# Kernel tuning notes

Measured on AMD Instinct MI355X. Metric: run time of the kernel, lower is better.

Reference implementation:

```python
import jax, jax.numpy as jnp
import numpy as np

IN_FEATURES = 4096
OUT_FEATURES = 768
N_BITS = 8
BATCH = 4096


def setup_inputs() -> dict:
    key = jax.random.key(0)
    k1, k2, k3 = jax.random.split(key, 3)
    latent = jax.random.uniform(k1, (BATCH, IN_FEATURES), dtype=jnp.float32)
    true_sum = jax.random.uniform(k2, (BATCH, OUT_FEATURES * N_BITS), dtype=jnp.float32)
    # kaiming-normal-ish init: std = sqrt(2 / fan_in)
    weight = jax.random.normal(k3, (IN_FEATURES, OUT_FEATURES * N_BITS), dtype=jnp.float32) * np.sqrt(2.0 / IN_FEATURES)
    return {"latent": latent, "true_sum": true_sum, "weight": weight, "n_bits": N_BITS}


def reference(latent, true_sum, weight, n_bits):
    in_features = weight.shape[0]
    batch = latent.shape[0]
    # powers of two, MSB negated (two's-complement style decode)
    powers = (2.0 ** jnp.arange(n_bits, dtype=jnp.float32))
    powers = powers.at[-1].multiply(-1.0)

    prob_weights = jax.nn.sigmoid(weight)                      # [in, out*n_bits]
    # decode soft bits -> integer-valued weights: [in, out]
    int_weights = (prob_weights.reshape(in_features, -1, n_bits) * powers).sum(-1)
    # decode target bits -> integer-valued sums: [batch, out]
    int_sum = (true_sum.reshape(batch, -1, n_bits) * powers).sum(-1)

    # (latent.unsqueeze(-1) * int_weights).sum(-2) is exactly a GEMM
    pred = latent @ int_weights                                # [batch, out]

    scale_factor = 2.0 ** (n_bits - 1)
    recon_loss = jnp.mean((pred - int_sum) ** 2) / scale_factor
    polarize_loss = jnp.mean(prob_weights * (1.0 - prob_weights))
    return (recon_loss, polarize_loss)
```

## Files before the change

kernel.cpp:

```cpp
#include <hip/hip_runtime.h>
#include <stdint.h>

#define IN_F   4096
#define OUT_F  768
#define NB     8
#define BATCH  4096
#define WCOLS  (OUT_F*NB)

typedef short  bf16x8  __attribute__((ext_vector_type(8)));
typedef float  f32x4   __attribute__((ext_vector_type(4)));
typedef unsigned short ushort8 __attribute__((ext_vector_type(8)));

__device__ __forceinline__ unsigned short f2bf(float f){
    union { float f; uint32_t u; } v; v.f = f;
    uint32_t u = v.u;
    u += 0x7FFFu + ((u >> 16) & 1u);
    return (unsigned short)(u >> 16);
}

__device__ __forceinline__ float bf2f(unsigned short u){
    union { uint32_t q; float f; } v; v.q = ((uint32_t)u) << 16;
    return v.f;
}

__device__ __forceinline__ void gload16(const void* g, void* l){
    __builtin_amdgcn_global_load_lds(
        (const __attribute__((address_space(1))) unsigned int*)g,
        (__attribute__((address_space(3))) unsigned int*)l, 16, 0, 0);
}

#define WAITV(n) do {                                                   \
    asm volatile("s_waitcnt vmcnt(" #n ")" ::: "memory");               \
    __builtin_amdgcn_sched_barrier(0);                                  \
} while (0)

__global__ void prep_latent(const float* __restrict__ lat,
                            unsigned short* __restrict__ abf,
                            float* __restrict__ acc){
    if (blockIdx.x == 0 && threadIdx.x < 4) acc[threadIdx.x] = 0.f;
    int idx = (blockIdx.x * 256 + threadIdx.x) * 8;
    const float4* p = (const float4*)(lat + idx);
    float4 a = p[0], b = p[1];
    ushort8 o;
    o[0]=f2bf(a.x); o[1]=f2bf(a.y); o[2]=f2bf(a.z); o[3]=f2bf(a.w);
    o[4]=f2bf(b.x); o[5]=f2bf(b.y); o[6]=f2bf(b.z); o[7]=f2bf(b.w);
    *(ushort8*)(abf + idx) = o;
}

__global__ void decode_weight(const float* __restrict__ w,
                              unsigned short* __restrict__ bt,
                              float* __restrict__ acc){
    __shared__ unsigned short tile[64][70];
    __shared__ float part[4];
    const int tid = threadIdx.x;
    const int k0 = blockIdx.x * 64;
    const int n0 = blockIdx.y * 64;
    const int j     = tid & 63;
    const int ibase = (tid >> 6) * 16;
    float pol = 0.f;
    #pragma unroll 4
    for (int r = 0; r < 16; ++r){
        int i = ibase + r;
        const float4* src = (const float4*)(w + (size_t)(k0+i)*WCOLS + (size_t)(n0+j)*8);
        float4 a = src[0], b = src[1];
        float x[8] = {a.x,a.y,a.z,a.w,b.x,b.y,b.z,b.w};
        float p[8];
        #pragma unroll
        for (int q = 0; q < 8; ++q){
            p[q] = 1.f / (1.f + __expf(-x[q]));
            pol += p[q] * (1.f - p[q]);
        }
        float iw = p[0] + 2.f*p[1] + 4.f*p[2] + 8.f*p[3]
                 + 16.f*p[4] + 32.f*p[5] + 64.f*p[6] - 128.f*p[7];
        tile[j][i] = f2bf(iw);
    }
    #pragma unroll
    for (int off = 32; off; off >>= 1) pol += __shfl_down(pol, off);
    if ((tid & 63) == 0) part[tid >> 6] = pol;
    __syncthreads();
    const int nrow = tid >> 4;
    const int kb   = (tid & 15) * 4;
    #pragma unroll
    for (int q = 0; q < 4; ++q){
        int n = nrow + q*16;
        uint2 v;
        v.x = *(const unsigned int*)&tile[n][kb];
        v.y = *(const unsigned int*)&tile[n][kb+2];
        *(uint2*)(bt + (size_t)(n0+n)*IN_F + k0 + kb) = v;
    }
    if (tid == 0) atomicAdd(&acc[1], part[0]+part[1]+part[2]+part[3]);
}

__global__ void ts_decode(const float* __restrict__ ts,
                          unsigned short* __restrict__ isum){
    const int tid = threadIdx.x;
    #pragma unroll
    for (int k = 0; k < 6; ++k){
        int e = blockIdx.x * 1536 + k * 256 + tid;
        const float4* q = (const float4*)(ts + (size_t)e * 8);
        float4 x = q[0], y = q[1];
        float v = x.x + 2.f*x.y + 4.f*x.z + 8.f*x.w
                + 16.f*y.x + 32.f*y.y + 64.f*y.z - 128.f*y.w;
        isum[e] = f2bf(v);
    }
}

#define BM 64
#define BN 96
#define BK 64
#define NT (IN_F/BK)
#define ABYTES (BM*BK*2)
#define BBYTES (BN*BK*2)
#define BUFB   (ABYTES+BBYTES)

__launch_bounds__(512, 4)
__global__ void gemm_loss(const unsigned short* __restrict__ abf,
                          const unsigned short* __restrict__ bt,
                          const unsigned short* __restrict__ isum,
                          float* __restrict__ acc){
    __shared__ char smem[3*BUFB];
    __shared__ float part[8];
    const int tid = threadIdx.x;
    const int w   = tid >> 6;
    const int l   = tid & 63;
    const int s   = l & 15, g = l >> 4;
    const int wr  = w >> 1, wc = w & 1;
    const int bid = blockIdx.x;
    const int m0  = (bid >> 3) * BM;
    const int n0  = (bid & 7)  * BN;

    f32x4 accv[2][3];
    #pragma unroll
    for (int m = 0; m < 2; ++m)
        #pragma unroll
        for (int n = 0; n < 3; ++n)
            accv[m][n] = (f32x4){0.f,0.f,0.f,0.f};

    #define COMPUTE(base) do {                                             \
        char* _Ab = (base);                                                \
        char* _Bb = (base) + ABYTES;                                       \
        _Pragma("unroll")                                                  \
        for (int _kk = 0; _kk < 2; ++_kk){                                 \
            bf16x8 _af[2], _bf[3];                                         \
            _Pragma("unroll")                                              \
            for (int _m = 0; _m < 2; ++_m){                                \
                int _r  = wr*32 + _m*16 + s;                               \
                int _ch = _r*8 + ((_kk*4 + g) ^ (_r & 7));                 \
                _af[_m] = *(const bf16x8*)(_Ab + _ch*16);                  \
            }                                                              \
            _Pragma("unroll")                                              \
            for (int _n = 0; _n < 3; ++_n){                                \
                int _r  = wc*48 + _n*16 + s;                               \
                int _ch = _r*8 + ((_kk*4 + g) ^ (_r & 7));                 \
                _bf[_n] = *(const bf16x8*)(_Bb + _ch*16);                  \
            }                                                              \
            __builtin_amdgcn_s_setprio(1);                                 \
            _Pragma("unroll")                                              \
            for (int _m = 0; _m < 2; ++_m)                                 \
                _Pragma("unroll")                                          \
                for (int _n = 0; _n < 3; ++_n)                             \
                    accv[_m][_n] = __builtin_amdgcn_mfma_f32_16x16x32_bf16(\
                        _af[_m], _bf[_n], accv[_m][_n], 0, 0, 0);          \
            __builtin_amdgcn_s_setprio(0);                                 \
        }                                                                  \
    } while (0)

    char* r0 = smem;
    char* r1 = smem + BUFB;
    char* r2 = smem + 2*BUFB;

    if (w >= 4){
        const int p  = w - 4;
        const int lr = l >> 3;
        const int lc = l & 7;
        const unsigned short* src[5];
        int dsto[5];
        #pragma unroll
        for (int i = 0; i < 5; ++i){
            int c   = p + 4*i;
            int row = (c < 8) ? (c*8 + lr) : ((c-8)*8 + lr);
            int csw = ((lc ^ (row & 7)) << 3);
            src[i]  = (c < 8) ? (abf + (size_t)(m0 + row)*IN_F + csw)
                              : (bt  + (size_t)(n0 + row)*IN_F + csw);
            dsto[i] = c * 1024;
        }
        #define STAGEP(kt, base) do {                                     \
            _Pragma("unroll")                                             \
            for (int _i = 0; _i < 5; ++_i)                                \
                gload16(src[_i] + (size_t)(kt)*BK, (base) + dsto[_i]);    \
        } while (0)

        STAGEP(0, r0);
        STAGEP(1, r1);
        WAITV(5);
        __builtin_amdgcn_s_barrier();
        for (int t = 0; t < NT; ++t){
            __builtin_amdgcn_sched_barrier(0);
            if (t < NT-2)      { STAGEP(t+2, r2); WAITV(5); }
            else if (t == NT-2){ WAITV(0); }
            __builtin_amdgcn_s_barrier();
            char* tmp = r0; r0 = r1; r1 = r2; r2 = tmp;
        }
    } else {
        __builtin_amdgcn_s_barrier();
        for (int t = 0; t < NT; ++t){
            __builtin_amdgcn_sched_barrier(0);
            COMPUTE(r0);
            __builtin_amdgcn_sched_barrier(0);
            __builtin_amdgcn_s_barrier();
            char* tmp = r0; r0 = r1; r1 = r2; r2 = tmp;
        }
    }

    float local = 0.f;
    if (w < 4){
        #pragma unroll
        for (int m = 0; m < 2; ++m){
            int rbase = m0 + wr*32 + m*16 + g*4;
            #pragma unroll
            for (int n = 0; n < 3; ++n){
                int col = n0 + wc*48 + n*16 + s;
                #pragma unroll
                for (int jj = 0; jj < 4; ++jj){
                    float is = bf2f(isum[(size_t)(rbase+jj)*OUT_F + col]);
                    float d = accv[m][n][jj] - is;
                    local += d*d;
                }
            }
        }
    }
    #pragma unroll
    for (int off = 32; off; off >>= 1) local += __shfl_down(local, off);
    if (l == 0) part[w] = local;
    __syncthreads();
    if (tid == 0){
        float ssum = 0.f;
        #pragma unroll
        for (int i = 0; i < 8; ++i) ssum += part[i];
        atomicAdd(&acc[0], ssum);
    }
}

__global__ void finalize(const float* __restrict__ acc, float* __restrict__ out){
    out[0] = acc[0] * (1.0f / ((float)BATCH * (float)OUT_F * 128.0f));
    out[1] = acc[1] * (1.0f / ((float)IN_F * (float)WCOLS));
}

extern "C" void kernel_launch(void* const* d_in, const int* in_sizes, int n_in,
                              void* d_out, int out_size, void* d_ws, size_t ws_size,
                              hipStream_t stream){
    const float* latent   = (const float*)d_in[0];
    const float* true_sum = (const float*)d_in[1];
    const float* weight   = (const float*)d_in[2];
    float* acc = (float*)d_ws;
    unsigned short* abf  = (unsigned short*)((char*)d_ws + 1024);
    unsigned short* bt   = (unsigned short*)((char*)d_ws + 1024 + (size_t)BATCH*IN_F*2);
    unsigned short* isum = (unsigned short*)((char*)d_ws + 1024 + (size_t)BATCH*IN_F*2
                                             + (size_t)OUT_F*IN_F*2);
    float* out = (float*)d_out;

    prep_latent<<<(BATCH*IN_F)/(256*8), 256, 0, stream>>>(latent, abf, acc);
    decode_weight<<<dim3(IN_F/64, OUT_F/64), 256, 0, stream>>>(weight, bt, acc);
    ts_decode<<<(BATCH*OUT_F)/(256*6), 256, 0, stream>>>(true_sum, isum);
    gemm_loss<<<BATCH/BM * OUT_F/BN, 512, 0, stream>>>(abf, bt, isum, acc);
    finalize<<<1, 1, 0, stream>>>(acc, out);
}
```

Before: 109.0 us.

## Fuse latent bf16 conversion into GEMM producer warps and merge decode kernels

```diff
diff --git a/kernel.cpp b/kernel.cpp
--- a/kernel.cpp
+++ b/kernel.cpp
@@ -9,7 +9,6 @@
 
 typedef short  bf16x8  __attribute__((ext_vector_type(8)));
 typedef float  f32x4   __attribute__((ext_vector_type(4)));
-typedef unsigned short ushort8 __attribute__((ext_vector_type(8)));
 
 __device__ __forceinline__ unsigned short f2bf(float f){
     union { float f; uint32_t u; } v; v.f = f;
@@ -34,74 +33,66 @@
     __builtin_amdgcn_sched_barrier(0);                                  \
 } while (0)
 
-__global__ void prep_latent(const float* __restrict__ lat,
-                            unsigned short* __restrict__ abf,
-                            float* __restrict__ acc){
-    if (blockIdx.x == 0 && threadIdx.x < 4) acc[threadIdx.x] = 0.f;
-    int idx = (blockIdx.x * 256 + threadIdx.x) * 8;
-    const float4* p = (const float4*)(lat + idx);
-    float4 a = p[0], b = p[1];
-    ushort8 o;
-    o[0]=f2bf(a.x); o[1]=f2bf(a.y); o[2]=f2bf(a.z); o[3]=f2bf(a.w);
-    o[4]=f2bf(b.x); o[5]=f2bf(b.y); o[6]=f2bf(b.z); o[7]=f2bf(b.w);
-    *(ushort8*)(abf + idx) = o;
-}
-
-__global__ void decode_weight(const float* __restrict__ w,
-                              unsigned short* __restrict__ bt,
-                              float* __restrict__ acc){
+#define LGKM0() asm volatile("s_waitcnt lgkmcnt(0)" ::: "memory")
+
+__launch_bounds__(256)
+__global__ void decode_all(const float* __restrict__ w,
+                           const float* __restrict__ ts,
+                           unsigned short* __restrict__ bt,
+                           unsigned short* __restrict__ isum,
+                           float* __restrict__ polp){
     __shared__ unsigned short tile[64][70];
     __shared__ float part[4];
     const int tid = threadIdx.x;
-    const int k0 = blockIdx.x * 64;
-    const int n0 = blockIdx.y * 64;
-    const int j     = tid & 63;
-    const int ibase = (tid >> 6) * 16;
-    float pol = 0.f;
-    #pragma unroll 4
-    for (int r = 0; r < 16; ++r){
-        int i = ibase + r;
-        const float4* src = (const float4*)(w + (size_t)(k0+i)*WCOLS + (size_t)(n0+j)*8);
-        float4 a = src[0], b = src[1];
-        float x[8] = {a.x,a.y,a.z,a.w,b.x,b.y,b.z,b.w};
-        float p[8];
-        #pragma unroll
-        for (int q = 0; q < 8; ++q){
-            p[q] = 1.f / (1.f + __expf(-x[q]));
-            pol += p[q] * (1.f - p[q]);
-        }
-        float iw = p[0] + 2.f*p[1] + 4.f*p[2] + 8.f*p[3]
-                 + 16.f*p[4] + 32.f*p[5] + 64.f*p[6] - 128.f*p[7];
-        tile[j][i] = f2bf(iw);
-    }
-    #pragma unroll
-    for (int off = 32; off; off >>= 1) pol += __shfl_down(pol, off);
-    if ((tid & 63) == 0) part[tid >> 6] = pol;
-    __syncthreads();
-    const int nrow = tid >> 4;
-    const int kb   = (tid & 15) * 4;
-    #pragma unroll
-    for (int q = 0; q < 4; ++q){
-        int n = nrow + q*16;
-        uint2 v;
-        v.x = *(const unsigned int*)&tile[n][kb];
-        v.y = *(const unsigned int*)&tile[n][kb+2];
-        *(uint2*)(bt + (size_t)(n0+n)*IN_F + k0 + kb) = v;
-    }
-    if (tid == 0) atomicAdd(&acc[1], part[0]+part[1]+part[2]+part[3]);
-}
-
-__global__ void ts_decode(const float* __restrict__ ts,
-                          unsigned short* __restrict__ isum){
-    const int tid = threadIdx.x;
-    #pragma unroll
-    for (int k = 0; k < 6; ++k){
-        int e = blockIdx.x * 1536 + k * 256 + tid;
-        const float4* q = (const float4*)(ts + (size_t)e * 8);
-        float4 x = q[0], y = q[1];
-        float v = x.x + 2.f*x.y + 4.f*x.z + 8.f*x.w
-                + 16.f*y.x + 32.f*y.y + 64.f*y.z - 128.f*y.w;
-        isum[e] = f2bf(v);
+    const int bid = blockIdx.x;
+    if (bid < 768){
+        const int k0 = (bid & 63) * 64;
+        const int n0 = (bid >> 6) * 64;
+        const int j     = tid & 63;
+        const int ibase = (tid >> 6) * 16;
+        float pol = 0.f;
+        #pragma unroll 4
+        for (int r = 0; r < 16; ++r){
+            int i = ibase + r;
+            const float4* src = (const float4*)(w + (size_t)(k0+i)*WCOLS + (size_t)(n0+j)*8);
+            float4 a = src[0], b = src[1];
+            float x[8] = {a.x,a.y,a.z,a.w,b.x,b.y,b.z,b.w};
+            float p[8];
+            #pragma unroll
+            for (int q = 0; q < 8; ++q){
+                p[q] = 1.f / (1.f + __expf(-x[q]));
+                pol += p[q] * (1.f - p[q]);
+            }
+            float iw = p[0] + 2.f*p[1] + 4.f*p[2] + 8.f*p[3]
+                     + 16.f*p[4] + 32.f*p[5] + 64.f*p[6] - 128.f*p[7];
+            tile[j][i] = f2bf(iw);
+        }
+        #pragma unroll
+        for (int off = 32; off; off >>= 1) pol += __shfl_down(pol, off);
+        if ((tid & 63) == 0) part[tid >> 6] = pol;
+        __syncthreads();
+        const int nrow = tid >> 4;
+        const int kb   = (tid & 15) * 4;
+        #pragma unroll
+        for (int q = 0; q < 4; ++q){
+            int n = nrow + q*16;
+            uint2 v;
+            v.x = *(const unsigned int*)&tile[n][kb];
+            v.y = *(const unsigned int*)&tile[n][kb+2];
+            *(uint2*)(bt + (size_t)(n0+n)*IN_F + k0 + kb) = v;
+        }
+        if (tid == 0) polp[bid] = part[0]+part[1]+part[2]+part[3];
+    } else {
+        const int b = bid - 768;
+        #pragma unroll
+        for (int k = 0; k < 6; ++k){
+            int e = b * 1536 + k * 256 + tid;
+            const float4* q = (const float4*)(ts + (size_t)e * 8);
+            float4 x = q[0], y = q[1];
+            float v = x.x + 2.f*x.y + 4.f*x.z + 8.f*x.w
+                    + 16.f*y.x + 32.f*y.y + 64.f*y.z - 128.f*y.w;
+            isum[e] = f2bf(v);
+        }
     }
 }
 
@@ -109,111 +100,77 @@
 #define BN 96
 #define BK 64
 #define NT (IN_F/BK)
-#define ABYTES (BM*BK*2)
+#define A_STRIDE 144
+#define ABYTES (BM*A_STRIDE)
 #define BBYTES (BN*BK*2)
 #define BUFB   (ABYTES+BBYTES)
 
 __launch_bounds__(512, 4)
-__global__ void gemm_loss(const unsigned short* __restrict__ abf,
+__global__ void gemm_loss(const float* __restrict__ lat,
                           const unsigned short* __restrict__ bt,
                           const unsigned short* __restrict__ isum,
-                          float* __restrict__ acc){
-    __shared__ char smem[3*BUFB];
+                          float* __restrict__ lossp){
+    __shared__ __align__(16) char smem[3*BUFB];
     __shared__ float part[8];
     const int tid = threadIdx.x;
     const int w   = tid >> 6;
     const int l   = tid & 63;
     const int s   = l & 15, g = l >> 4;
-    const int wr  = w >> 1, wc = w & 1;
     const int bid = blockIdx.x;
-    const int m0  = (bid >> 3) * BM;
-    const int n0  = (bid & 7)  * BN;
-
-    f32x4 accv[2][3];
-    #pragma unroll
-    for (int m = 0; m < 2; ++m)
-        #pragma unroll
-        for (int n = 0; n < 3; ++n)
-            accv[m][n] = (f32x4){0.f,0.f,0.f,0.f};
-
-    #define COMPUTE(base) do {                                             \
-        char* _Ab = (base);                                                \
-        char* _Bb = (base) + ABYTES;                                       \
-        _Pragma("unroll")                                                  \
-        for (int _kk = 0; _kk < 2; ++_kk){                                 \
-            bf16x8 _af[2], _bf[3];                                         \
-            _Pragma("unroll")                                              \
-            for (int _m = 0; _m < 2; ++_m){                                \
-                int _r  = wr*32 + _m*16 + s;                               \
-                int _ch = _r*8 + ((_kk*4 + g) ^ (_r & 7));                 \
-                _af[_m] = *(const bf16x8*)(_Ab + _ch*16);                  \
-            }                                                              \
-            _Pragma("unroll")                                              \
-            for (int _n = 0; _n < 3; ++_n){                                \
-                int _r  = wc*48 + _n*16 + s;                               \
-                int _ch = _r*8 + ((_kk*4 + g) ^ (_r & 7));                 \
-                _bf[_n] = *(const bf16x8*)(_Bb + _ch*16);                  \
-            }                                                              \
-            __builtin_amdgcn_s_setprio(1);                                 \
-            _Pragma("unroll")                                              \
-            for (int _m = 0; _m < 2; ++_m)                                 \
-                _Pragma("unroll")                                          \
-                for (int _n = 0; _n < 3; ++_n)                             \
-                    accv[_m][_n] = __builtin_amdgcn_mfma_f32_16x16x32_bf16(\
-                        _af[_m], _bf[_n], accv[_m][_n], 0, 0, 0);          \
-            __builtin_amdgcn_s_setprio(0);                                 \
-        }                                                                  \
-    } while (0)
+    const int m0  = (bid & 63) * BM;
+    const int n0  = (bid >> 6) * BN;
 
     char* r0 = smem;
     char* r1 = smem + BUFB;
     char* r2 = smem + 2*BUFB;
-
-    if (w >= 4){
-        const int p  = w - 4;
-        const int lr = l >> 3;
-        const int lc = l & 7;
-        const unsigned short* src[5];
-        int dsto[5];
-        #pragma unroll
-        for (int i = 0; i < 5; ++i){
-            int c   = p + 4*i;
-            int row = (c < 8) ? (c*8 + lr) : ((c-8)*8 + lr);
-            int csw = ((lc ^ (row & 7)) << 3);
-            src[i]  = (c < 8) ? (abf + (size_t)(m0 + row)*IN_F + csw)
-                              : (bt  + (size_t)(n0 + row)*IN_F + csw);
-            dsto[i] = c * 1024;
-        }
-        #define STAGEP(kt, base) do {                                     \
-            _Pragma("unroll")                                             \
-            for (int _i = 0; _i < 5; ++_i)                                \
-                gload16(src[_i] + (size_t)(kt)*BK, (base) + dsto[_i]);    \
+    #define ROT() do { char* _t = r0; r0 = r1; r1 = r2; r2 = _t; } while (0)
+
+    float local = 0.f;
+
+    if (w < 4){
+        const int wr = w >> 1, wc = w & 1;
+        f32x4 accv[2][3];
+        #pragma unroll
+        for (int m = 0; m < 2; ++m)
+            #pragma unroll
+            for (int n = 0; n < 3; ++n)
+                accv[m][n] = (f32x4){0.f,0.f,0.f,0.f};
+
+        #define COMPUTE(base) do {                                             \
+            char* _Ab = (base);                                                \
+            char* _Bb = (base) + ABYTES;                                       \
+            _Pragma("unroll")                                                  \
+            for (int _kk = 0; _kk < 2; ++_kk){                                 \
+                bf16x8 _af[2], _bf[3];                                         \
+                _Pragma("unroll")                                              \
+                for (int _m = 0; _m < 2; ++_m){                                \
+                    int _r  = wr*32 + _m*16 + s;                               \
+                    _af[_m] = *(const bf16x8*)(_Ab + _r*A_STRIDE               \
+                                               + (_kk*4 + g)*16);              \
+                }                                                              \
+                _Pragma("unroll")                                              \
+                for (int _n = 0; _n < 3; ++_n){                                \
+                    int _r  = wc*48 + _n*16 + s;                               \
+                    int _ch = _r*8 + ((_kk*4 + g) ^ (_r & 7));                 \
+                    _bf[_n] = *(const bf16x8*)(_Bb + _ch*16);                  \
+                }                                                              \
+                __builtin_amdgcn_s_setprio(1);                                 \
+                _Pragma("unroll")                                              \
+                for (int _m = 0; _m < 2; ++_m)                                 \
+                    _Pragma("unroll")                                          \
+                    for (int _n = 0; _n < 3; ++_n)                             \
+                        accv[_m][_n] = __builtin_amdgcn_mfma_f32_16x16x32_bf16(\
+                            _af[_m], _bf[_n], accv[_m][_n], 0, 0, 0);          \
+                __builtin_amdgcn_s_setprio(0);                                 \
+            }                                                                  \
         } while (0)
 
-        STAGEP(0, r0);
-        STAGEP(1, r1);
-        WAITV(5);
         __builtin_amdgcn_s_barrier();
         for (int t = 0; t < NT; ++t){
-            __builtin_amdgcn_sched_barrier(0);
-            if (t < NT-2)      { STAGEP(t+2, r2); WAITV(5); }
-            else if (t == NT-2){ WAITV(0); }
+            COMPUTE(r0);
             __builtin_amdgcn_s_barrier();
-            char* tmp = r0; r0 = r1; r1 = r2; r2 = tmp;
-        }
-    } else {
-        __builtin_amdgcn_s_barrier();
-        for (int t = 0; t < NT; ++t){
-            __builtin_amdgcn_sched_barrier(0);
-            COMPUTE(r0);
-            __builtin_amdgcn_sched_barrier(0);
-            __builtin_amdgcn_s_barrier();
-            char* tmp = r0; r0 = r1; r1 = r2; r2 = tmp;
-        }
-    }
-
-    float local = 0.f;
-    if (w < 4){
+            ROT();
+        }
         #pragma unroll
         for (int m = 0; m < 2; ++m){
             int rbase = m0 + wr*32 + m*16 + g*4;
@@ -228,7 +185,86 @@
                 }
             }
         }
-    }
+    } else if (w < 6){
+        const int p  = w - 4;
+        const int lr = l >> 3;
+        const int lc = l & 7;
+        #define BSTAGE(kt, base) do {                                          \
+            _Pragma("unroll")                                                  \
+            for (int _i = 0; _i < 6; ++_i){                                    \
+                int _c   = p*6 + _i;                                           \
+                int _row = _c*8 + lr;                                          \
+                int _csw = ((lc ^ (_row & 7)) << 3);                           \
+                gload16(bt + (size_t)(n0 + _row)*IN_F + _csw + (size_t)(kt)*BK,\
+                        (base) + ABYTES + _c*1024);                            \
+            }                                                                  \
+        } while (0)
+
+        BSTAGE(0, r0); BSTAGE(1, r1);
+        WAITV(6);
+        __builtin_amdgcn_s_barrier();
+        for (int t = 0; t < NT; ++t){
+            if (t + 2 < NT) { BSTAGE(t+2, r2); WAITV(6); }
+            else if (t == NT-2) { WAITV(0); }
+            __builtin_amdgcn_s_barrier();
+            ROT();
+        }
+    } else {
+        const int ar = (w - 6)*32 + (l >> 1);
+        const int ah = l & 1;
+        const float* aSrc = lat + (size_t)(m0 + ar)*IN_F + ah*32;
+        const int   aOff  = ar*A_STRIDE + ah*64;
+
+        f32x4 sA0[8], sA1[8];
+        #define AISSUE(kt, SET) do {                                           \
+            const f32x4* _p = (const f32x4*)(aSrc + (size_t)(kt)*BK);          \
+            _Pragma("unroll")                                                  \
+            for (int _j = 0; _j < 8; ++_j) SET[_j] = _p[_j];                   \
+        } while (0)
+
+        #define ACOMMIT(SET, dstbuf) do {                                      \
+            uint32_t _wd[16];                                                  \
+            _Pragma("unroll")                                                  \
+            for (int _j = 0; _j < 16; ++_j){                                   \
+                float _lo = SET[_j >> 1][2*(_j & 1)];                          \
+                float _hi = SET[_j >> 1][2*(_j & 1) + 1];                      \
+                asm("v_cvt_pk_bf16_f32 %0, %1, %2"                             \
+                    : "=v"(_wd[_j]) : "v"(_lo), "v"(_hi));                     \
+            }                                                                  \
+            char* _d = (dstbuf) + aOff;                                        \
+            _Pragma("unroll")                                                  \
+            for (int _q = 0; _q < 4; ++_q)                                     \
+                *(int4*)(_d + _q*16) = *(const int4*)&_wd[_q*4];               \
+        } while (0)
+
+        AISSUE(0, sA0); AISSUE(1, sA1);
+        WAITV(8);
+        ACOMMIT(sA0, r0);
+        LGKM0();
+        __builtin_amdgcn_s_barrier();
+        for (int tp = 0; tp < 31; ++tp){
+            AISSUE(2*tp + 2, sA0);
+            WAITV(8);
+            ACOMMIT(sA1, r1);
+            LGKM0();
+            __builtin_amdgcn_s_barrier();
+            ROT();
+            AISSUE(2*tp + 3, sA1);
+            WAITV(8);
+            ACOMMIT(sA0, r1);
+            LGKM0();
+            __builtin_amdgcn_s_barrier();
+            ROT();
+        }
+        WAITV(0);
+        ACOMMIT(sA1, r1);
+        LGKM0();
+        __builtin_amdgcn_s_barrier();
+        ROT();
+        __builtin_amdgcn_s_barrier();
+        ROT();
+    }
+
     #pragma unroll
     for (int off = 32; off; off >>= 1) local += __shfl_down(local, off);
     if (l == 0) part[w] = local;
@@ -237,13 +273,34 @@
         float ssum = 0.f;
         #pragma unroll
         for (int i = 0; i < 8; ++i) ssum += part[i];
-        atomicAdd(&acc[0], ssum);
-    }
-}
-
-__global__ void finalize(const float* __restrict__ acc, float* __restrict__ out){
-    out[0] = acc[0] * (1.0f / ((float)BATCH * (float)OUT_F * 128.0f));
-    out[1] = acc[1] * (1.0f / ((float)IN_F * (float)WCOLS));
+        lossp[bid] = ssum;
+    }
+}
+
+__launch_bounds__(256)
+__global__ void finalize(const float* __restrict__ lossp,
+                         const float* __restrict__ polp,
+                         float* __restrict__ out){
+    __shared__ float sm[2][4];
+    const int tid = threadIdx.x;
+    float a = 0.f, b = 0.f;
+    #pragma unroll
+    for (int i = tid; i < 512; i += 256) a += lossp[i];
+    #pragma unroll
+    for (int i = tid; i < 768; i += 256) b += polp[i];
+    #pragma unroll
+    for (int off = 32; off; off >>= 1){
+        a += __shfl_down(a, off);
+        b += __shfl_down(b, off);
+    }
+    if ((tid & 63) == 0){ sm[0][tid >> 6] = a; sm[1][tid >> 6] = b; }
+    __syncthreads();
+    if (tid == 0){
+        float sa = sm[0][0]+sm[0][1]+sm[0][2]+sm[0][3];
+        float sb = sm[1][0]+sm[1][1]+sm[1][2]+sm[1][3];
+        out[0] = sa * (1.0f / ((float)BATCH * (float)OUT_F * 128.0f));
+        out[1] = sb * (1.0f / ((float)IN_F * (float)WCOLS));
+    }
 }
 
 extern "C" void kernel_launch(void* const* d_in, const int* in_sizes, int n_in,
@@ -252,16 +309,14 @@
     const float* latent   = (const float*)d_in[0];
     const float* true_sum = (const float*)d_in[1];
     const float* weight   = (const float*)d_in[2];
-    float* acc = (float*)d_ws;
-    unsigned short* abf  = (unsigned short*)((char*)d_ws + 1024);
-    unsigned short* bt   = (unsigned short*)((char*)d_ws + 1024 + (size_t)BATCH*IN_F*2);
-    unsigned short* isum = (unsigned short*)((char*)d_ws + 1024 + (size_t)BATCH*IN_F*2
+    float* lossp = (float*)d_ws;
+    float* polp  = (float*)((char*)d_ws + 4096);
+    unsigned short* bt   = (unsigned short*)((char*)d_ws + 16384);
+    unsigned short* isum = (unsigned short*)((char*)d_ws + 16384
                                              + (size_t)OUT_F*IN_F*2);
     float* out = (float*)d_out;
 
-    prep_latent<<<(BATCH*IN_F)/(256*8), 256, 0, stream>>>(latent, abf, acc);
-    decode_weight<<<dim3(IN_F/64, OUT_F/64), 256, 0, stream>>>(weight, bt, acc);
-    ts_decode<<<(BATCH*OUT_F)/(256*6), 256, 0, stream>>>(true_sum, isum);
-    gemm_loss<<<BATCH/BM * OUT_F/BN, 512, 0, stream>>>(abf, bt, isum, acc);
-    finalize<<<1, 1, 0, stream>>>(acc, out);
-}
+    decode_all<<<768 + 2048, 256, 0, stream>>>(weight, true_sum, bt, isum, polp);
+    gemm_loss<<<(BATCH/BM)*(OUT_F/BN), 512, 0, stream>>>(latent, bt, isum, lossp);
+    finalize<<<1, 256, 0, stream>>>(lossp, polp, out);
+}
```

Measured after the change: 113.7 us. +4.3%, slower.
